# Performance work log

Measured on AMD Instinct MI355X. Metric: run time of the kernel, lower is better.

## Reference

```python
import jax, jax.numpy as jnp
import numpy as np

INPUT_DIM = 1024
NUM_TARGETS = 128
BATCH = 32768


def setup_inputs() -> dict:
    key = jax.random.key(0)
    kx, kw, kb = jax.random.split(key, 3)
    x = jax.random.normal(kx, (BATCH, INPUT_DIM), dtype=jnp.float32)
    # Fused view of num_targets independent nn.Linear(input_dim, 1) layers:
    # column t of W / entry t of b are the weights/bias of layer t.
    bound = 1.0 / np.sqrt(INPUT_DIM)  # torch Linear default init range
    W = jax.random.uniform(kw, (INPUT_DIM, NUM_TARGETS), minval=-bound, maxval=bound, dtype=jnp.float32)
    b = jax.random.uniform(kb, (NUM_TARGETS,), minval=-bound, maxval=bound, dtype=jnp.float32)
    return {"x": x, "W": W, "b": b}


def reference(x, W, b):
    # Equivalent to concatenating sigmoid(Linear_t(x)) over t along last dim:
    # one fused matmul [B,D]x[D,T] + bias + sigmoid.
    return jax.nn.sigmoid(x @ W + b)
```

## Files before the change

kernel.cpp:

```cpp
#include <hip/hip_runtime.h>
#include <hip/hip_bf16.h>


typedef __bf16 bf16x8 __attribute__((ext_vector_type(8)));
typedef float  f32x4  __attribute__((ext_vector_type(4)));

#define DIM   1024
#define NT    128
#define BATCH 32768

__global__ __launch_bounds__(256) void prep_w(const float* __restrict__ W,
                                              __bf16* __restrict__ wsW) {
    int idx = blockIdx.x * 256 + threadIdx.x;
    int j = idx & 7;
    int l = (idx >> 3) & 63;
    int c = (idx >> 9) & 7;
    int s = idx >> 12;
    int k = s * 32 + (l >> 4) * 8 + j;
    int n = c * 16 + (l & 15);
    wsW[idx] = (__bf16)W[k * NT + n];
}

__device__ __forceinline__ bf16x8 cvt_bf16x8(float4 a0, float4 a1) {
    bf16x8 af;
    af[0] = (__bf16)a0.x; af[1] = (__bf16)a0.y;
    af[2] = (__bf16)a0.z; af[3] = (__bf16)a0.w;
    af[4] = (__bf16)a1.x; af[5] = (__bf16)a1.y;
    af[6] = (__bf16)a1.z; af[7] = (__bf16)a1.w;
    return af;
}

__global__ __launch_bounds__(256) void gemm_bias_sigmoid(
        const float* __restrict__ x,
        const __hip_bfloat16* __restrict__ wsWh,
        const float* __restrict__ bias,
        float* __restrict__ out) {
    const bf16x8* __restrict__ wsW8 = (const bf16x8*)wsWh;
    __shared__ bf16x8 ldsW[4096];

    const int tid  = threadIdx.x;
    const int lane = tid & 63;
    const int wave = tid >> 6;
    const int q    = lane >> 4;
    const int r    = lane & 15;
    const int row0 = blockIdx.x * 64 + wave * 16;

    const float* xA = x + (size_t)(row0 + r) * DIM + q * 8;

    f32x4 acc[8];
#pragma unroll
    for (int c = 0; c < 8; ++c)
        acc[c] = (f32x4){0.f, 0.f, 0.f, 0.f};

    float4 S0[8], S1[8];

#pragma unroll
    for (int i = 0; i < 4; ++i) {
        const float* ap = xA + (size_t)i * 32;
        S0[2 * i]     = *(const float4*)ap;
        S0[2 * i + 1] = *(const float4*)(ap + 4);
    }

    for (int p = 0; p < 4; ++p) {
        __syncthreads();
#pragma unroll
        for (int i = 0; i < 16; ++i) {
            const int e = tid + i * 256;
            ldsW[e] = wsW8[p * 4096 + e];
        }
#pragma unroll
        for (int i = 0; i < 4; ++i) {
            const float* ap = xA + (size_t)(p * 8 + 4 + i) * 32;
            S1[2 * i]     = *(const float4*)ap;
            S1[2 * i + 1] = *(const float4*)(ap + 4);
        }
        __syncthreads();

#pragma unroll
        for (int sl = 0; sl < 4; ++sl) {
            const bf16x8 af = cvt_bf16x8(S0[2 * sl], S0[2 * sl + 1]);
#pragma unroll
            for (int c = 0; c < 8; ++c) {
                const bf16x8 bf = ldsW[(sl * 8 + c) * 64 + lane];
                acc[c] = __builtin_amdgcn_mfma_f32_16x16x32_bf16(af, bf, acc[c], 0, 0, 0);
            }
        }
        if (p < 3) {
#pragma unroll
            for (int i = 0; i < 4; ++i) {
                const float* ap = xA + (size_t)((p + 1) * 8 + i) * 32;
                S0[2 * i]     = *(const float4*)ap;
                S0[2 * i + 1] = *(const float4*)(ap + 4);
            }
        }
#pragma unroll
        for (int sl = 4; sl < 8; ++sl) {
            const bf16x8 af = cvt_bf16x8(S1[2 * (sl - 4)], S1[2 * (sl - 4) + 1]);
#pragma unroll
            for (int c = 0; c < 8; ++c) {
                const bf16x8 bf = ldsW[(sl * 8 + c) * 64 + lane];
                acc[c] = __builtin_amdgcn_mfma_f32_16x16x32_bf16(af, bf, acc[c], 0, 0, 0);
            }
        }
    }

#pragma unroll
    for (int c = 0; c < 8; ++c) {
        const float bv = bias[c * 16 + r];
#pragma unroll
        for (int reg = 0; reg < 4; ++reg) {
            const int row = row0 + q * 4 + reg;
            float v = acc[c][reg] + bv;
            v = 1.0f / (1.0f + __expf(-v));
            out[(size_t)row * NT + c * 16 + r] = v;
        }
    }
}

extern "C" void kernel_launch(void* const* d_in, const int* in_sizes, int n_in,
                              void* d_out, int out_size, void* d_ws, size_t ws_size,
                              hipStream_t stream) {
    const float* x = (const float*)d_in[0];
    const float* W = (const float*)d_in[1];
    const float* b = (const float*)d_in[2];
    float* out     = (float*)d_out;
    __bf16* wsW    = (__bf16*)d_ws;

    prep_w<<<DIM * NT / 256, 256, 0, stream>>>(W, wsW);
    gemm_bias_sigmoid<<<BATCH / 64, 256, 0, stream>>>(
        x, (const __hip_bfloat16*)wsW, b, out);
}
```

Measured before the change: 203.5 us.

## Double block size and W staging chunk, use rolling 4-deep x prefetch

```diff
diff --git a/kernel.cpp b/kernel.cpp
--- a/kernel.cpp
+++ b/kernel.cpp
@@ -30,20 +30,20 @@
     return af;
 }
 
-__global__ __launch_bounds__(256) void gemm_bias_sigmoid(
+__global__ __launch_bounds__(512, 2) void gemm_bias_sigmoid(
         const float* __restrict__ x,
         const __hip_bfloat16* __restrict__ wsWh,
         const float* __restrict__ bias,
         float* __restrict__ out) {
     const bf16x8* __restrict__ wsW8 = (const bf16x8*)wsWh;
-    __shared__ bf16x8 ldsW[4096];
+    __shared__ bf16x8 ldsW[8192];
 
     const int tid  = threadIdx.x;
     const int lane = tid & 63;
     const int wave = tid >> 6;
     const int q    = lane >> 4;
     const int r    = lane & 15;
-    const int row0 = blockIdx.x * 64 + wave * 16;
+    const int row0 = blockIdx.x * 128 + wave * 16;
 
     const float* xA = x + (size_t)(row0 + r) * DIM + q * 8;
 
@@ -52,50 +52,39 @@
     for (int c = 0; c < 8; ++c)
         acc[c] = (f32x4){0.f, 0.f, 0.f, 0.f};
 
-    float4 S0[8], S1[8];
+    float4 A[4][2];
+#pragma unroll
+    for (int i = 0; i < 4; ++i) {
+        A[i][0] = *(const float4*)(xA + (size_t)i * 32);
+        A[i][1] = *(const float4*)(xA + (size_t)i * 32 + 4);
+    }
 
 #pragma unroll
-    for (int i = 0; i < 4; ++i) {
-        const float* ap = xA + (size_t)i * 32;
-        S0[2 * i]     = *(const float4*)ap;
-        S0[2 * i + 1] = *(const float4*)(ap + 4);
-    }
+    for (int i = 0; i < 16; ++i)
+        ldsW[tid + i * 512] = wsW8[tid + i * 512];
+    __syncthreads();
 
-    for (int p = 0; p < 4; ++p) {
-        __syncthreads();
 #pragma unroll
-        for (int i = 0; i < 16; ++i) {
-            const int e = tid + i * 256;
-            ldsW[e] = wsW8[p * 4096 + e];
+    for (int h = 0; h < 2; ++h) {
+        if (h == 1) {
+            __syncthreads();
+#pragma unroll
+            for (int i = 0; i < 16; ++i)
+                ldsW[tid + i * 512] = wsW8[8192 + tid + i * 512];
+            __syncthreads();
         }
 #pragma unroll
-        for (int i = 0; i < 4; ++i) {
-            const float* ap = xA + (size_t)(p * 8 + 4 + i) * 32;
-            S1[2 * i]     = *(const float4*)ap;
-            S1[2 * i + 1] = *(const float4*)(ap + 4);
-        }
-        __syncthreads();
+        for (int sl = 0; sl < 16; ++sl) {
+            const int s   = h * 16 + sl;
+            const int buf = s & 3;
 
-#pragma unroll
-        for (int sl = 0; sl < 4; ++sl) {
-            const bf16x8 af = cvt_bf16x8(S0[2 * sl], S0[2 * sl + 1]);
-#pragma unroll
-            for (int c = 0; c < 8; ++c) {
-                const bf16x8 bf = ldsW[(sl * 8 + c) * 64 + lane];
-                acc[c] = __builtin_amdgcn_mfma_f32_16x16x32_bf16(af, bf, acc[c], 0, 0, 0);
+            const bf16x8 af = cvt_bf16x8(A[buf][0], A[buf][1]);
+
+            if (s + 4 < 32) {
+                A[buf][0] = *(const float4*)(xA + (size_t)(s + 4) * 32);
+                A[buf][1] = *(const float4*)(xA + (size_t)(s + 4) * 32 + 4);
             }
-        }
-        if (p < 3) {
-#pragma unroll
-            for (int i = 0; i < 4; ++i) {
-                const float* ap = xA + (size_t)((p + 1) * 8 + i) * 32;
-                S0[2 * i]     = *(const float4*)ap;
-                S0[2 * i + 1] = *(const float4*)(ap + 4);
-            }
-        }
-#pragma unroll
-        for (int sl = 4; sl < 8; ++sl) {
-            const bf16x8 af = cvt_bf16x8(S1[2 * (sl - 4)], S1[2 * (sl - 4) + 1]);
+
 #pragma unroll
             for (int c = 0; c < 8; ++c) {
                 const bf16x8 bf = ldsW[(sl * 8 + c) * 64 + lane];
@@ -127,6 +116,6 @@
     __bf16* wsW    = (__bf16*)d_ws;
 
     prep_w<<<DIM * NT / 256, 256, 0, stream>>>(W, wsW);
-    gemm_bias_sigmoid<<<BATCH / 64, 256, 0, stream>>>(
+    gemm_bias_sigmoid<<<BATCH / 128, 512, 0, stream>>>(
         x, (const __hip_bfloat16*)wsW, b, out);
 }
```

After: 211.8 us. 4.1% more time.

## Double-buffer W and x tiles in LDS with async global_load_lds

Applied to the files above, without the earlier changes.

```diff
diff --git a/kernel.cpp b/kernel.cpp
--- a/kernel.cpp
+++ b/kernel.cpp
@@ -3,11 +3,18 @@
 
 
 typedef __bf16 bf16x8 __attribute__((ext_vector_type(8)));
+typedef __bf16 bf16x4 __attribute__((ext_vector_type(4)));
 typedef float  f32x4  __attribute__((ext_vector_type(4)));
+typedef unsigned int u32_as1 __attribute__((address_space(1)));
+typedef unsigned int u32_as3 __attribute__((address_space(3)));
 
 #define DIM   1024
 #define NT    128
 #define BATCH 32768
+
+#define LDS_BYTES 50176
+#define A_OFS     32768u
+#define A_STRIDE  136u
 
 __global__ __launch_bounds__(256) void prep_w(const float* __restrict__ W,
                                               __bf16* __restrict__ wsW) {
@@ -21,95 +28,106 @@
     wsW[idx] = (__bf16)W[k * NT + n];
 }
 
-__device__ __forceinline__ bf16x8 cvt_bf16x8(float4 a0, float4 a1) {
-    bf16x8 af;
-    af[0] = (__bf16)a0.x; af[1] = (__bf16)a0.y;
-    af[2] = (__bf16)a0.z; af[3] = (__bf16)a0.w;
-    af[4] = (__bf16)a1.x; af[5] = (__bf16)a1.y;
-    af[6] = (__bf16)a1.z; af[7] = (__bf16)a1.w;
-    return af;
-}
-
 __global__ __launch_bounds__(256) void gemm_bias_sigmoid(
         const float* __restrict__ x,
         const __hip_bfloat16* __restrict__ wsWh,
         const float* __restrict__ bias,
         float* __restrict__ out) {
+    __shared__ __align__(16) unsigned char lds[LDS_BYTES];
     const bf16x8* __restrict__ wsW8 = (const bf16x8*)wsWh;
-    __shared__ bf16x8 ldsW[4096];
 
     const int tid  = threadIdx.x;
     const int lane = tid & 63;
     const int wave = tid >> 6;
     const int q    = lane >> 4;
     const int r    = lane & 15;
-    const int row0 = blockIdx.x * 64 + wave * 16;
+    const int row0 = blockIdx.x * 64;
 
-    const float* xA = x + (size_t)(row0 + r) * DIM + q * 8;
+    const int rbase = tid >> 4;
+    const int kk4   = (tid & 15) * 4;
 
     f32x4 acc[8];
 #pragma unroll
     for (int c = 0; c < 8; ++c)
         acc[c] = (f32x4){0.f, 0.f, 0.f, 0.f};
 
-    float4 S0[8], S1[8];
+    float4 areg[4];
 
 #pragma unroll
     for (int i = 0; i < 4; ++i) {
-        const float* ap = xA + (size_t)i * 32;
-        S0[2 * i]     = *(const float4*)ap;
-        S0[2 * i + 1] = *(const float4*)(ap + 4);
+        const bf16x8* g = wsW8 + (i * 256 + tid);
+        __builtin_amdgcn_global_load_lds(
+            (const u32_as1*)g,
+            (u32_as3*)(lds + (unsigned)((i * 256 + wave * 64) * 16)),
+            16, 0, 0);
+    }
+#pragma unroll
+    for (int i = 0; i < 4; ++i)
+        areg[i] = *(const float4*)(x + (size_t)(row0 + rbase + i * 16) * DIM + kk4);
+#pragma unroll
+    for (int i = 0; i < 4; ++i) {
+        bf16x4 v;
+        v[0] = (__bf16)areg[i].x; v[1] = (__bf16)areg[i].y;
+        v[2] = (__bf16)areg[i].z; v[3] = (__bf16)areg[i].w;
+        *(bf16x4*)(lds + A_OFS + (unsigned)(rbase + i * 16) * A_STRIDE + (unsigned)kk4 * 2) = v;
+    }
+    __syncthreads();
+
+#pragma unroll
+    for (int c = 0; c < 16; ++c) {
+        const int cur = c & 1;
+        const int nxt = cur ^ 1;
+        const unsigned Wc = 16384u * (unsigned)cur;
+        const unsigned Ac = A_OFS + 8704u * (unsigned)cur;
+
+        if (c < 15) {
+#pragma unroll
+            for (int i = 0; i < 4; ++i) {
+                const bf16x8* g = wsW8 + ((c + 1) * 1024 + i * 256 + tid);
+                __builtin_amdgcn_global_load_lds(
+                    (const u32_as1*)g,
+                    (u32_as3*)(lds + 16384u * (unsigned)nxt +
+                               (unsigned)((i * 256 + wave * 64) * 16)),
+                    16, 0, 0);
+            }
+#pragma unroll
+            for (int i = 0; i < 4; ++i)
+                areg[i] = *(const float4*)(x + (size_t)(row0 + rbase + i * 16) * DIM +
+                                           (c + 1) * 64 + kk4);
+        }
+
+#pragma unroll
+        for (int sl = 0; sl < 2; ++sl) {
+            const bf16x8 af = *(const bf16x8*)(lds + Ac +
+                (unsigned)(wave * 16 + r) * A_STRIDE + (unsigned)(sl * 64 + q * 16));
+#pragma unroll
+            for (int cc = 0; cc < 8; ++cc) {
+                const bf16x8 bf = *(const bf16x8*)(lds + Wc +
+                    (unsigned)(((sl * 8 + cc) * 64 + lane) * 16));
+                acc[cc] = __builtin_amdgcn_mfma_f32_16x16x32_bf16(af, bf, acc[cc], 0, 0, 0);
+            }
+        }
+
+        if (c < 15) {
+#pragma unroll
+            for (int i = 0; i < 4; ++i) {
+                bf16x4 v;
+                v[0] = (__bf16)areg[i].x; v[1] = (__bf16)areg[i].y;
+                v[2] = (__bf16)areg[i].z; v[3] = (__bf16)areg[i].w;
+                *(bf16x4*)(lds + A_OFS + 8704u * (unsigned)nxt +
+                           (unsigned)(rbase + i * 16) * A_STRIDE + (unsigned)kk4 * 2) = v;
+            }
+        }
+        __syncthreads();
     }
 
-    for (int p = 0; p < 4; ++p) {
-        __syncthreads();
-#pragma unroll
-        for (int i = 0; i < 16; ++i) {
-            const int e = tid + i * 256;
-            ldsW[e] = wsW8[p * 4096 + e];
-        }
-#pragma unroll
-        for (int i = 0; i < 4; ++i) {
-            const float* ap = xA + (size_t)(p * 8 + 4 + i) * 32;
-            S1[2 * i]     = *(const float4*)ap;
-            S1[2 * i + 1] = *(const float4*)(ap + 4);
-        }
-        __syncthreads();
-
-#pragma unroll
-        for (int sl = 0; sl < 4; ++sl) {
-            const bf16x8 af = cvt_bf16x8(S0[2 * sl], S0[2 * sl + 1]);
-#pragma unroll
-            for (int c = 0; c < 8; ++c) {
-                const bf16x8 bf = ldsW[(sl * 8 + c) * 64 + lane];
-                acc[c] = __builtin_amdgcn_mfma_f32_16x16x32_bf16(af, bf, acc[c], 0, 0, 0);
-            }
-        }
-        if (p < 3) {
-#pragma unroll
-            for (int i = 0; i < 4; ++i) {
-                const float* ap = xA + (size_t)((p + 1) * 8 + i) * 32;
-                S0[2 * i]     = *(const float4*)ap;
-                S0[2 * i + 1] = *(const float4*)(ap + 4);
-            }
-        }
-#pragma unroll
-        for (int sl = 4; sl < 8; ++sl) {
-            const bf16x8 af = cvt_bf16x8(S1[2 * (sl - 4)], S1[2 * (sl - 4) + 1]);
-#pragma unroll
-            for (int c = 0; c < 8; ++c) {
-                const bf16x8 bf = ldsW[(sl * 8 + c) * 64 + lane];
-                acc[c] = __builtin_amdgcn_mfma_f32_16x16x32_bf16(af, bf, acc[c], 0, 0, 0);
-            }
-        }
-    }
-
+    const int wrow = row0 + wave * 16;
 #pragma unroll
     for (int c = 0; c < 8; ++c) {
         const float bv = bias[c * 16 + r];
 #pragma unroll
         for (int reg = 0; reg < 4; ++reg) {
-            const int row = row0 + q * 4 + reg;
+            const int row = wrow + q * 4 + reg;
             float v = acc[c][reg] + bv;
             v = 1.0f / (1.0f + __expf(-v));
             out[(size_t)row * NT + c * 16 + r] = v;
```

Result: slower. 210.3 us (+3.4%).
